# Kernel tuning notes

Measured on AMD Instinct MI355X. Metric: run time of the kernel, lower is better.

## Reference

```python
import jax, jax.numpy as jnp
import numpy as np

N_SU = 8
DATA_DIM = N_SU * N_SU - 1  # 63
BATCH = 1048576


def _gell_mann(n):
    """Generalized Gell-Mann matrices of su(n), Tr(L_a L_b) = 2 delta_ab."""
    mats = []
    for j in range(n):
        for k in range(j + 1, n):
            m = np.zeros((n, n), dtype=np.complex128); m[j, k] = 1.0; m[k, j] = 1.0
            mats.append(m)
            m = np.zeros((n, n), dtype=np.complex128); m[j, k] = -1.0j; m[k, j] = 1.0j
            mats.append(m)
    for l in range(1, n):
        m = np.zeros((n, n), dtype=np.complex128)
        c = np.sqrt(2.0 / (l * (l + 1)))
        for j in range(l):
            m[j, j] = c
        m[l, l] = -l * c
        mats.append(m)
    return np.stack(mats)


def _structure_const(n):
    """f_abc = Tr([L_a,L_b]L_c)/(4i), d_abc = Tr({L_a,L_b}L_c)/4 (both real)."""
    L = _gell_mann(n)                                  # (D, n, n)
    P = np.einsum('aij,bjk->abik', L, L)               # L_a L_b
    comm = P - P.transpose(1, 0, 2, 3)
    anti = P + P.transpose(1, 0, 2, 3)
    f = (np.einsum('abik,cki->abc', comm, L) / 4.0j).real
    d = (np.einsum('abik,cki->abc', anti, L) / 4.0).real
    return f.astype(np.float32), d.astype(np.float32)

F_CONST, D_CONST = _structure_const(N_SU)              # (D, D, D) each, compile-time constants
TRI = np.stack(np.triu_indices(DATA_DIM, 0))           # incl. diagonal
TRI1 = np.stack(np.triu_indices(DATA_DIM, 1))          # strict upper


def setup_inputs() -> dict:
    key = jax.random.key(0)
    k1, k2, k3, k4, k5 = jax.random.split(key, 5)
    D = DATA_DIM
    return {
        'x': jax.random.normal(k1, (BATCH, D), dtype=jnp.float32),
        'r_x': jax.random.uniform(k2, (D * (D + 1) // 2,), dtype=jnp.float32),
        'r_y': jax.random.uniform(k3, (D * (D - 1) // 2,), dtype=jnp.float32),
        'N': jax.random.uniform(k4, (1,), dtype=jnp.float32),
        'omega': jax.random.uniform(k5, (D,), dtype=jnp.float32),
    }


def _forward(x, r_x, r_y, N, omega):
    f = jnp.asarray(F_CONST)
    d = jnp.asarray(D_CONST)
    D = DATA_DIM
    # NOTE: faithful to the torch source, where `v_x = v_y = torch.zeros(...)`
    # aliases ONE tensor: r_y overwrites r_x on the strict upper triangle and
    # v_x is v_y, which makes c_im exactly zero.
    v = jnp.zeros((D, D), dtype=x.dtype)
    v = v.at[TRI[0], TRI[1]].set(r_x)
    v = v.at[TRI1[0], TRI1[1]].set(r_y)
    v_x = v
    v_y = v
    c_re = v_x.T @ v_x + v_y.T @ v_y                   # einsum('ki,kj->ij', v, v) x2
    c_re = c_re / jnp.trace(c_re)
    c_im = v_x.T @ v_y - v_y.T @ v_x                   # exactly zero (aliasing)
    c_re = N * c_re

    # Precompute the small (D,D) superoperator coefficient matrices once, then
    # apply them to the batch with plain matmuls (bn,mn->bm).
    A1 = jnp.einsum('mjk,ij->mik', f, c_re)
    M_re1 = jnp.einsum('mik,nik->mn', A1, f)           # 'mjk,nik,ij->mn'
    A2 = jnp.einsum('mik,ij->mjk', f, c_re)
    M_re2 = jnp.einsum('mjk,njk->mn', A2, f)           # 'mik,njk,ij->mn'
    B1 = jnp.einsum('mjk,ij->mik', f, c_im)
    M_im1 = jnp.einsum('mik,nik->mn', B1, d)
    B2 = jnp.einsum('mik,ij->mjk', f, c_im)
    M_im2 = jnp.einsum('mjk,njk->mn', B2, d)
    M = -2.0 * M_re1 - 2.0 * M_re2 - 2.0 * M_im1 + 2.0 * M_im2

    d_super_x = x @ M.T                                 # (B, D)
    H = 8.0 * jnp.einsum('kij,k->ij', f, omega)
    h_commutator_x = x @ H.T                            # 'kij,k,bj->bi'
    tr_id = -8.0 * jnp.einsum('imj,ij->m', f, c_im)     # (D,), zero here

    S_x = h_commutator_x + d_super_x
    T_x = x + tr_id
    L_x = S_x + T_x
    return x + 0.01 * L_x


def reference(x, r_x, r_y, N, omega):
    return _forward(x, r_x, r_y, N, omega)
```

## Files before the change

### kernel.cpp

```cpp
#include <hip/hip_runtime.h>

#define DD 63
#define DD2 (DD * DD)
#define NSU 8

typedef __attribute__((ext_vector_type(8))) short short8;
typedef __attribute__((ext_vector_type(4))) float f32x4;

__device__ float  g_F[DD2 * DD];
__device__ float  g_B[DD * DD2];
__device__ float  g_cc[DD2];
__device__ float  g_scale;
__device__ unsigned short g_Gtb[64 * 64];

__device__ __forceinline__ unsigned short f2bf(float f) {
    union { float f; unsigned u; } v; v.f = f;
    unsigned r = v.u + 0x7FFFu + ((v.u >> 16) & 1u);
    return (unsigned short)(r >> 16);
}

__device__ __forceinline__ void fill_L(int a, float (*re)[NSU], float (*im)[NSU]) {
    if (a < 56) {
        int p = a >> 1;
        int j = 0, rem = p;
        while (rem >= 7 - j) { rem -= 7 - j; ++j; }
        int k = j + 1 + rem;
        if ((a & 1) == 0) { re[j][k] = 1.f; re[k][j] = 1.f; }
        else             { im[j][k] = -1.f; im[k][j] = 1.f; }
    } else {
        int l = a - 55;
        float c = sqrtf(2.f / (float)(l * (l + 1)));
        for (int j = 0; j < l; ++j) re[j][j] = c;
        re[l][l] = -(float)l * c;
    }
}

__global__ __launch_bounds__(256) void setup_kernel(const float* __restrict__ r_x,
                                                    const float* __restrict__ r_y,
                                                    const float* __restrict__ Np) {
    const int t = threadIdx.x;
    if (blockIdx.x < DD) {
        const int a = blockIdx.x;
        __shared__ float Ar[NSU][NSU], Ai[NSU][NSU];
        __shared__ float Br[4][NSU][NSU], Bi[4][NSU][NSU];
        __shared__ float Cr[4][NSU][NSU], Ci[4][NSU][NSU];
        const int w = t >> 6, lane = t & 63;
        const int r = lane >> 3, c = lane & 7;
        if (t < 64) { Ar[r][c] = 0.f; Ai[r][c] = 0.f; }
        __syncthreads();
        if (t == 0) fill_L(a, Ar, Ai);
        __syncthreads();
        for (int rb = 0; rb < 16; ++rb) {
            const int b = rb * 4 + w;
            const bool act = (b < DD);
            if (act) { Br[w][r][c] = 0.f; Bi[w][r][c] = 0.f; }
            __syncthreads();
            if (act && lane == 0) fill_L(b, Br[w], Bi[w]);
            __syncthreads();
            if (act) {
                float pr = 0.f, pi = 0.f, qr = 0.f, qi = 0.f;
                #pragma unroll
                for (int k = 0; k < NSU; ++k) {
                    pr += Ar[r][k] * Br[w][k][c] - Ai[r][k] * Bi[w][k][c];
                    pi += Ar[r][k] * Bi[w][k][c] + Ai[r][k] * Br[w][k][c];
                    qr += Br[w][r][k] * Ar[k][c] - Bi[w][r][k] * Ai[k][c];
                    qi += Br[w][r][k] * Ai[k][c] + Bi[w][r][k] * Ar[k][c];
                }
                Cr[w][r][c] = pr - qr;
                Ci[w][r][c] = pi - qi;
            }
            __syncthreads();
            if (act && lane < DD) {
                float im;
                if (lane < 56) {
                    int p = lane >> 1;
                    int j = 0, rem = p;
                    while (rem >= 7 - j) { rem -= 7 - j; ++j; }
                    int k = j + 1 + rem;
                    if ((lane & 1) == 0) im = Ci[w][j][k] + Ci[w][k][j];
                    else                 im = Cr[w][j][k] - Cr[w][k][j];
                } else {
                    int l = lane - 55;
                    float cd = sqrtf(2.f / (float)(l * (l + 1)));
                    float s = 0.f;
                    for (int j = 0; j < l; ++j) s += Ci[w][j][j];
                    im = cd * s - (float)l * cd * Ci[w][l][l];
                }
                g_F[(a * DD + b) * DD + lane] = 0.25f * im;
            }
            __syncthreads();
        }
    } else {
        __shared__ float v[DD2];
        __shared__ float ccs[DD2];
        for (int idx = t; idx < DD2; idx += 256) {
            int i = idx / DD, j = idx % DD;
            float val = 0.f;
            if (j > i)       val = r_y[62 * i - (i * (i - 1)) / 2 + (j - i - 1)];
            else if (j == i) val = r_x[63 * i - (i * (i - 1)) / 2];
            v[idx] = val;
        }
        __syncthreads();
        for (int idx = t; idx < DD2; idx += 256) {
            int i = idx / DD, j = idx % DD;
            float s = 0.f;
            for (int k = 0; k < DD; ++k) s = fmaf(v[k * DD + i], v[k * DD + j], s);
            ccs[idx] = s;
            g_cc[idx] = s;
        }
        __syncthreads();
        if (t == 0) {
            float tr = 0.f;
            for (int i = 0; i < DD; ++i) tr += ccs[i * DD + i];
            g_scale = Np[0] / tr;
        }
    }
}

__global__ __launch_bounds__(256) void buildB_kernel() {
    __shared__ float scc[DD2];
    __shared__ float sf[DD2];
    const int t = threadIdx.x;
    const int n = blockIdx.x;
    for (int idx = t; idx < DD2; idx += 256) {
        scc[idx] = g_cc[idx];
        sf[idx]  = g_F[n * DD2 + idx];
    }
    __syncthreads();
    for (int idx = t; idx < DD2; idx += 256) {
        const int j = idx / DD, k = idx % DD;
        float s = 0.f;
        for (int i = 0; i < DD; ++i) s = fmaf(scc[i * DD + j], sf[i * DD + k], s);
        g_B[n * DD2 + idx] = s;
    }
}

__global__ __launch_bounds__(64) void buildKt_kernel(const float* __restrict__ omega) {
    const int m = blockIdx.x >> 6;
    const int n = blockIdx.x & 63;
    const int lane = threadIdx.x;
    if (m >= DD || n >= DD) {
        if (lane == 0) g_Gtb[n * 64 + m] = 0;
        return;
    }
    const float* __restrict__ Fm = g_F + m * DD2;
    const float* __restrict__ Bn = g_B + n * DD2;
    float p = 0.f;
    for (int idx = lane; idx < DD2; idx += 64) p = fmaf(Fm[idx], Bn[idx], p);
    float h = (lane < DD) ? g_F[lane * DD2 + m * DD + n] * omega[lane] : 0.f;
    #pragma unroll
    for (int off = 32; off > 0; off >>= 1) {
        p += __shfl_down(p, off);
        h += __shfl_down(h, off);
    }
    if (lane == 0)
        g_Gtb[n * 64 + m] = f2bf(0.01f * (-4.f * g_scale * p + 8.f * h));
}

__global__ __launch_bounds__(256) void apply_kernel(const float* __restrict__ x,
                                                    float* __restrict__ out) {
    __shared__ __align__(16) float tile[256 * DD + 16];
    __shared__ __align__(16) unsigned short sG[64 * 64];
    const int t = threadIdx.x;
    const size_t base = (size_t)blockIdx.x * (256 * DD);

    const float4* __restrict__ gsrc = (const float4*)(x + base);
    float4* __restrict__ ltile = (float4*)tile;
    #pragma unroll
    for (int it = 0; it < 16; ++it) {
        int idx = t + it * 256;
        if (idx < 4032) ltile[idx] = gsrc[idx];
    }
    const int* __restrict__ gG = (const int*)g_Gtb;
    int* __restrict__ lG = (int*)sG;
    #pragma unroll
    for (int it = 0; it < 8; ++it) lG[t + it * 256] = gG[t + it * 256];
    __syncthreads();

    const int w = t >> 6, lane = t & 63;
    const int mrow = lane & 15;
    const int q = lane >> 4;

    short8 bfrag[2][4];
    #pragma unroll
    for (int kt = 0; kt < 2; ++kt)
        #pragma unroll
        for (int nt = 0; nt < 4; ++nt)
            #pragma unroll
            for (int j = 0; j < 8; ++j)
                bfrag[kt][nt][j] = (short)sG[(kt * 32 + q * 8 + j) * 64 + nt * 16 + mrow];

    #pragma unroll
    for (int mt = 0; mt < 4; ++mt) {
        const int row = w * 64 + mt * 16 + mrow;
        const float* __restrict__ ap = tile + row * DD;
        short8 af[2];
        #pragma unroll
        for (int kt = 0; kt < 2; ++kt)
            #pragma unroll
            for (int j = 0; j < 8; ++j)
                af[kt][j] = (short)f2bf(ap[kt * 32 + q * 8 + j]);

        f32x4 acc[4] = {{0.f,0.f,0.f,0.f},{0.f,0.f,0.f,0.f},
                        {0.f,0.f,0.f,0.f},{0.f,0.f,0.f,0.f}};
        #pragma unroll
        for (int nt = 0; nt < 4; ++nt) {
            acc[nt] = __builtin_amdgcn_mfma_f32_16x16x32_bf16(af[0], bfrag[0][nt], acc[nt], 0, 0, 0);
            acc[nt] = __builtin_amdgcn_mfma_f32_16x16x32_bf16(af[1], bfrag[1][nt], acc[nt], 0, 0, 0);
        }

        #pragma unroll
        for (int nt = 0; nt < 4; ++nt) {
            const int ocol = nt * 16 + mrow;
            if (ocol < DD) {
                #pragma unroll
                for (int r = 0; r < 4; ++r) {
                    const int orow = w * 64 + mt * 16 + q * 4 + r;
                    const int idx = orow * DD + ocol;
                    tile[idx] = 1.01f * tile[idx] + acc[nt][r];
                }
            }
        }
    }
    __syncthreads();

    float4* __restrict__ gdst = (float4*)(out + base);
    #pragma unroll
    for (int it = 0; it < 16; ++it) {
        int idx = t + it * 256;
        if (idx < 4032) gdst[idx] = ltile[idx];
    }
}

extern "C" void kernel_launch(void* const* d_in, const int* in_sizes, int n_in,
                              void* d_out, int out_size, void* d_ws, size_t ws_size,
                              hipStream_t stream) {
    const float* x     = (const float*)d_in[0];
    const float* r_x   = (const float*)d_in[1];
    const float* r_y   = (const float*)d_in[2];
    const float* Np    = (const float*)d_in[3];
    const float* omega = (const float*)d_in[4];
    float* out = (float*)d_out;

    const int rows = in_sizes[0] / DD;
    const int nblocks = rows / 256;

    setup_kernel<<<DD + 1, 256, 0, stream>>>(r_x, r_y, Np);
    buildB_kernel<<<DD, 256, 0, stream>>>();
    buildKt_kernel<<<64 * 64, 64, 0, stream>>>(omega);
    apply_kernel<<<nblocks, 256, 0, stream>>>(x, out);
}
```

Baseline: 196.5 us.

## Halve apply tile to 128 rows and vectorize B-fragment loads via transposed G

```diff
diff --git a/kernel.cpp b/kernel.cpp
--- a/kernel.cpp
+++ b/kernel.cpp
@@ -1,8 +1,10 @@
 #include <hip/hip_runtime.h>
+#include <hip/hip_bf16.h>
 
 #define DD 63
 #define DD2 (DD * DD)
 #define NSU 8
+#define TROWS 128
 
 typedef __attribute__((ext_vector_type(8))) short short8;
 typedef __attribute__((ext_vector_type(4))) float f32x4;
@@ -11,7 +13,7 @@
 __device__ float  g_B[DD * DD2];
 __device__ float  g_cc[DD2];
 __device__ float  g_scale;
-__device__ unsigned short g_Gtb[64 * 64];
+__device__ unsigned short g_Gb[64 * 64];
 
 __device__ __forceinline__ unsigned short f2bf(float f) {
     union { float f; unsigned u; } v; v.f = f;
@@ -140,7 +142,7 @@
     const int n = blockIdx.x & 63;
     const int lane = threadIdx.x;
     if (m >= DD || n >= DD) {
-        if (lane == 0) g_Gtb[n * 64 + m] = 0;
+        if (lane == 0) g_Gb[m * 64 + n] = 0;
         return;
     }
     const float* __restrict__ Fm = g_F + m * DD2;
@@ -154,27 +156,27 @@
         h += __shfl_down(h, off);
     }
     if (lane == 0)
-        g_Gtb[n * 64 + m] = f2bf(0.01f * (-4.f * g_scale * p + 8.f * h));
-}
-
-__global__ __launch_bounds__(256) void apply_kernel(const float* __restrict__ x,
-                                                    float* __restrict__ out) {
-    __shared__ __align__(16) float tile[256 * DD + 16];
+        g_Gb[m * 64 + n] = f2bf(0.01f * (-4.f * g_scale * p + 8.f * h));
+}
+
+__global__ __launch_bounds__(256, 4) void apply_kernel(const float* __restrict__ x,
+                                                       float* __restrict__ out) {
+    __shared__ __align__(16) float tile[TROWS * DD];
     __shared__ __align__(16) unsigned short sG[64 * 64];
     const int t = threadIdx.x;
-    const size_t base = (size_t)blockIdx.x * (256 * DD);
+    const size_t base = (size_t)blockIdx.x * (TROWS * DD);
 
     const float4* __restrict__ gsrc = (const float4*)(x + base);
     float4* __restrict__ ltile = (float4*)tile;
     #pragma unroll
-    for (int it = 0; it < 16; ++it) {
+    for (int it = 0; it < 8; ++it) {
         int idx = t + it * 256;
-        if (idx < 4032) ltile[idx] = gsrc[idx];
-    }
-    const int* __restrict__ gG = (const int*)g_Gtb;
-    int* __restrict__ lG = (int*)sG;
-    #pragma unroll
-    for (int it = 0; it < 8; ++it) lG[t + it * 256] = gG[t + it * 256];
+        if (idx < (TROWS * DD / 4)) ltile[idx] = gsrc[idx];
+    }
+    const int4* __restrict__ gG = (const int4*)g_Gb;
+    int4* __restrict__ lG = (int4*)sG;
+    lG[t]       = gG[t];
+    lG[t + 256] = gG[t + 256];
     __syncthreads();
 
     const int w = t >> 6, lane = t & 63;
@@ -186,20 +188,22 @@
     for (int kt = 0; kt < 2; ++kt)
         #pragma unroll
         for (int nt = 0; nt < 4; ++nt)
-            #pragma unroll
-            for (int j = 0; j < 8; ++j)
-                bfrag[kt][nt][j] = (short)sG[(kt * 32 + q * 8 + j) * 64 + nt * 16 + mrow];
-
-    #pragma unroll
-    for (int mt = 0; mt < 4; ++mt) {
-        const int row = w * 64 + mt * 16 + mrow;
+            bfrag[kt][nt] = *(const short8*)&sG[(nt * 16 + mrow) * 64 + kt * 32 + q * 8];
+
+    #pragma unroll
+    for (int mt = 0; mt < 2; ++mt) {
+        const int row = w * 32 + mt * 16 + mrow;
         const float* __restrict__ ap = tile + row * DD;
         short8 af[2];
         #pragma unroll
         for (int kt = 0; kt < 2; ++kt)
             #pragma unroll
-            for (int j = 0; j < 8; ++j)
-                af[kt][j] = (short)f2bf(ap[kt * 32 + q * 8 + j]);
+            for (int j = 0; j < 8; ++j) {
+                int k = kt * 32 + q * 8 + j;
+                float v = ap[(k == 63) ? 62 : k];
+                __hip_bfloat16 h = __float2bfloat16(v);
+                af[kt][j] = *reinterpret_cast<short*>(&h);
+            }
 
         f32x4 acc[4] = {{0.f,0.f,0.f,0.f},{0.f,0.f,0.f,0.f},
                         {0.f,0.f,0.f,0.f},{0.f,0.f,0.f,0.f}};
@@ -215,7 +219,7 @@
             if (ocol < DD) {
                 #pragma unroll
                 for (int r = 0; r < 4; ++r) {
-                    const int orow = w * 64 + mt * 16 + q * 4 + r;
+                    const int orow = w * 32 + mt * 16 + q * 4 + r;
                     const int idx = orow * DD + ocol;
                     tile[idx] = 1.01f * tile[idx] + acc[nt][r];
                 }
@@ -226,9 +230,9 @@
 
     float4* __restrict__ gdst = (float4*)(out + base);
     #pragma unroll
-    for (int it = 0; it < 16; ++it) {
+    for (int it = 0; it < 8; ++it) {
         int idx = t + it * 256;
-        if (idx < 4032) gdst[idx] = ltile[idx];
+        if (idx < (TROWS * DD / 4)) gdst[idx] = ltile[idx];
     }
 }
 
@@ -243,7 +247,7 @@
     float* out = (float*)d_out;
 
     const int rows = in_sizes[0] / DD;
-    const int nblocks = rows / 256;
+    const int nblocks = rows / TROWS;
 
     setup_kernel<<<DD + 1, 256, 0, stream>>>(r_x, r_y, Np);
     buildB_kernel<<<DD, 256, 0, stream>>>();
```

Result: faster. 183.8 us (-6.5%).
